# Optimization experiments

Measured on AMD Instinct MI355X. Metric: run time of the kernel, lower is better.

## Reference

```python
import jax, jax.numpy as jnp
import numpy as np

N = 100000
E = 1200000
C = 64
R = C // 8  # channel-attention reduced dim
G = 256    # number of graphs
EPS = 1e-5


def setup_inputs() -> dict:
    key = jax.random.key(0)
    ks = jax.random.split(key, 12)
    x = jax.random.normal(ks[0], (N, C), dtype=jnp.float32)
    edge_index = jax.random.randint(ks[1], (2, E), 0, N, dtype=jnp.int64)
    batch = jnp.sort(jax.random.randint(ks[2], (N,), 0, G, dtype=jnp.int64))
    s = 1.0 / np.sqrt(C)
    # SAGEConv: lin_l (applied to aggregated neighbors, with bias), lin_r (applied to self, no bias)
    Wl = jax.random.uniform(ks[3], (C, C), jnp.float32, -s, s)
    bl = jax.random.uniform(ks[4], (C,), jnp.float32, -s, s)
    Wr = jax.random.uniform(ks[5], (C, C), jnp.float32, -s, s)
    # GraphNorm params
    gn_w = jnp.ones((C,), jnp.float32)
    gn_b = jnp.zeros((C,), jnp.float32)
    gn_alpha = jnp.ones((C,), jnp.float32)  # mean_scale
    # ChannelAttention params
    sr = 1.0 / np.sqrt(C)
    a1_w = jax.random.uniform(ks[6], (R, C), jnp.float32, -sr, sr)
    a1_b = jax.random.uniform(ks[7], (R,), jnp.float32, -sr, sr)
    s2 = 1.0 / np.sqrt(R)
    a2_w = jax.random.uniform(ks[8], (C, R), jnp.float32, -s2, s2)
    a2_b = jax.random.uniform(ks[9], (C,), jnp.float32, -s2, s2)
    return {"x": x, "edge_index": edge_index, "batch": batch,
            "Wl": Wl, "bl": bl, "Wr": Wr,
            "gn_w": gn_w, "gn_b": gn_b, "gn_alpha": gn_alpha,
            "a1_w": a1_w, "a1_b": a1_b, "a2_w": a2_w, "a2_b": a2_b}


def _sage_conv(x, edge_index, Wl, bl, Wr):
    src, dst = edge_index[0], edge_index[1]
    # mean aggregation of neighbor features at destination nodes
    msg = x[src]  # [E, C]
    agg = jax.ops.segment_sum(msg, dst, num_segments=N)  # [N, C]
    deg = jax.ops.segment_sum(jnp.ones((E,), x.dtype), dst, num_segments=N)
    agg = agg / jnp.maximum(deg, 1.0)[:, None]
    return agg @ Wl.T + bl + x @ Wr.T


def _graph_norm(h, batch, w, b, alpha):
    cnt = jax.ops.segment_sum(jnp.ones((N,), h.dtype), batch, num_segments=G)
    cnt = jnp.maximum(cnt, 1.0)[:, None]  # [G,1]
    mean = jax.ops.segment_sum(h, batch, num_segments=G) / cnt  # [G,C]
    out = h - mean[batch] * alpha
    var = jax.ops.segment_sum(out * out, batch, num_segments=G) / cnt
    return w * out * jax.lax.rsqrt(var[batch] + EPS) + b


def reference(x, edge_index, batch, Wl, bl, Wr, gn_w, gn_b, gn_alpha,
              a1_w, a1_b, a2_w, a2_b):
    tmp = _graph_norm(_sage_conv(x, edge_index, Wl, bl, Wr), batch,
                      gn_w, gn_b, gn_alpha)
    # channel attention gate on the residual branch
    gate = jax.nn.sigmoid(jax.nn.relu(x @ a1_w.T + a1_b) @ a2_w.T + a2_b)
    tmp = tmp + gate * x
    # activation; dropout is identity at eval
    return jax.nn.relu(tmp)
```

## Files before the change

kernel.cpp:

```cpp
#include <hip/hip_runtime.h>
#include <math.h>

#define NN 100000
#define NE 1200000
#define CC 64
#define GG 256
#define RR 8
#define EPSF 1e-5f
#define BINS 782
#define BINP 1024
#define EPB 4688
#define QS 1028

__global__ __launch_bounds__(256) void k_hist(const int* __restrict__ ei,
                                              int* __restrict__ bin_total) {
  __shared__ int hist[BINP];
  for (int t = threadIdx.x; t < BINP; t += 256) hist[t] = 0;
  __syncthreads();
  int start = blockIdx.x * EPB;
  int end = start + EPB < NE ? start + EPB : NE;
  for (int e = start + threadIdx.x; e < end; e += 256)
    atomicAdd(&hist[ei[NE + e] >> 7], 1);
  __syncthreads();
  for (int t = threadIdx.x; t < BINP; t += 256)
    if (hist[t]) atomicAdd(&bin_total[t], hist[t]);
}

__global__ __launch_bounds__(1024) void k_scanbins(const int* __restrict__ bin_total,
                                                   int* __restrict__ bin_base,
                                                   int* __restrict__ cursor,
                                                   int* __restrict__ rowptr) {
  __shared__ int sh[BINP];
  int t = threadIdx.x;
  int v = t < BINS ? bin_total[t] : 0;
  sh[t] = v;
  __syncthreads();
  for (int d = 1; d < BINP; d <<= 1) {
    int val = sh[t];
    int add = (t >= d) ? sh[t - d] : 0;
    __syncthreads();
    sh[t] = val + add;
    __syncthreads();
  }
  int excl = sh[t] - v;
  if (t < BINS) {
    bin_base[t] = excl;
    cursor[t] = excl;
  }
  if (t == 0) {
    bin_base[BINS] = NE;
    rowptr[NN] = NE;
  }
}

__global__ __launch_bounds__(256) void k_phase1(const int* __restrict__ ei,
                                                int* __restrict__ cursor,
                                                unsigned* __restrict__ ebuf) {
  __shared__ int hist[BINP];
  __shared__ int base[BINP];
  for (int t = threadIdx.x; t < BINP; t += 256) hist[t] = 0;
  __syncthreads();
  int start = blockIdx.x * EPB;
  int end = start + EPB < NE ? start + EPB : NE;
  for (int e = start + threadIdx.x; e < end; e += 256)
    atomicAdd(&hist[ei[NE + e] >> 7], 1);
  __syncthreads();
  for (int t = threadIdx.x; t < BINP; t += 256) {
    int c = hist[t];
    base[t] = c ? atomicAdd(&cursor[t], c) : 0;
  }
  __syncthreads();
  for (int t = threadIdx.x; t < BINP; t += 256) hist[t] = 0;
  __syncthreads();
  for (int e = start + threadIdx.x; e < end; e += 256) {
    int src = ei[e], dst = ei[NE + e];
    int b = dst >> 7;
    int off = atomicAdd(&hist[b], 1);
    ebuf[base[b] + off] = ((unsigned)src << 7) | (unsigned)(dst & 127);
  }
}

__global__ __launch_bounds__(256) void k_fill2(const unsigned* __restrict__ ebuf,
                                               const int* __restrict__ bin_base,
                                               int* __restrict__ rowptr,
                                               int* __restrict__ csr) {
  __shared__ int cnt[128];
  __shared__ int sc[128];
  int tid = threadIdx.x;
  int b = blockIdx.x;
  int s = bin_base[b], e = bin_base[b + 1];
  if (tid < 128) cnt[tid] = 0;
  __syncthreads();
  for (int i = s + tid; i < e; i += 256) atomicAdd(&cnt[ebuf[i] & 127], 1);
  __syncthreads();
  if (tid < 128) sc[tid] = cnt[tid];
  __syncthreads();
  for (int d = 1; d < 128; d <<= 1) {
    int v = (tid < 128) ? sc[tid] : 0;
    int a = (tid >= d && tid < 128) ? sc[tid - d] : 0;
    __syncthreads();
    if (tid < 128) sc[tid] = v + a;
    __syncthreads();
  }
  if (tid < 128) {
    sc[tid] -= cnt[tid];
    int node = (b << 7) + tid;
    if (node < NN) rowptr[node] = s + sc[tid];
    cnt[tid] = 0;
  }
  __syncthreads();
  for (int i = s + tid; i < e; i += 256) {
    unsigned v = ebuf[i];
    int dl = v & 127;
    int off = atomicAdd(&cnt[dl], 1);
    csr[s + sc[dl] + off] = (int)(v >> 7);
  }
}

__global__ __launch_bounds__(256) void k_gather(const float* __restrict__ x,
                                                const int* __restrict__ csr,
                                                const int* __restrict__ rowptr,
                                                float* __restrict__ h) {
  int w = blockIdx.x * 4 + (threadIdx.x >> 6);
  int lane = threadIdx.x & 63;
  if (w >= NN) return;
  int s = rowptr[w], e = rowptr[w + 1];
  float acc = 0.0f;
  for (int j0 = s; j0 < e; j0 += 8) {
    int idx[8];
#pragma unroll
    for (int u = 0; u < 8; ++u) {
      int j = j0 + u;
      idx[u] = csr[j < e ? j : e - 1];
    }
    float v[8];
#pragma unroll
    for (int u = 0; u < 8; ++u) v[u] = x[(size_t)idx[u] * CC + lane];
#pragma unroll
    for (int u = 0; u < 8; ++u) acc += (j0 + u < e) ? v[u] : 0.0f;
  }
  h[(size_t)w * CC + lane] = acc;
}

__global__ __launch_bounds__(256) void k_passA(
    const float* __restrict__ x, float* h, const int* __restrict__ rowptr,
    const float* __restrict__ Wl, const float* __restrict__ bl,
    const float* __restrict__ Wr) {
  __shared__ float WLs[4 * QS];
  __shared__ float WRs[4 * QS];
  __shared__ float bls[CC];
  for (int idx = threadIdx.x; idx < CC * CC; idx += 256) {
    int c = idx >> 6, k = idx & 63;
    int qq = c >> 4, j = c & 15;
    WLs[qq * QS + j * 64 + k] = Wl[idx];
    WRs[qq * QS + j * 64 + k] = Wr[idx];
  }
  if (threadIdx.x < CC) bls[threadIdx.x] = bl[threadIdx.x];
  __syncthreads();

  int lane = threadIdx.x & 63;
  int wave = threadIdx.x >> 6;
  int n = lane & 15;
  int q = lane >> 4;
  int i0 = blockIdx.x * 256 + wave * 64 + n;
  const float4* wl = (const float4*)(WLs + q * QS);
  const float4* wr = (const float4*)(WRs + q * QS);

  const float4* ap[4];
  const float4* xp[4];
  float inv[4];
#pragma unroll
  for (int m = 0; m < 4; ++m) {
    int i = i0 + m * 16;
    int c = i < NN ? i : NN - 1;
    inv[m] = 1.0f / fmaxf((float)(rowptr[c + 1] - rowptr[c]), 1.0f);
    ap[m] = (const float4*)(h + (size_t)c * CC);
    xp[m] = (const float4*)(x + (size_t)c * CC);
  }

  float acc[4][16];
#pragma unroll
  for (int j = 0; j < 16; ++j) {
    float b = bls[q * 16 + j];
#pragma unroll
    for (int m = 0; m < 4; ++m) acc[m][j] = b;
  }

  for (int kbl = 0; kbl < 4; ++kbl) {
    float4 A[4][4];
#pragma unroll
    for (int m = 0; m < 4; ++m) {
#pragma unroll
      for (int t = 0; t < 4; ++t) {
        float4 v = ap[m][kbl * 4 + t];
        A[m][t] = make_float4(v.x * inv[m], v.y * inv[m], v.z * inv[m], v.w * inv[m]);
      }
    }
#pragma unroll
    for (int t = 0; t < 4; ++t) {
#pragma unroll
      for (int j = 0; j < 16; ++j) {
        float4 w = wl[j * 16 + kbl * 4 + t];
#pragma unroll
        for (int m = 0; m < 4; ++m) {
          float v = acc[m][j];
          v = fmaf(A[m][t].x, w.x, v);
          v = fmaf(A[m][t].y, w.y, v);
          v = fmaf(A[m][t].z, w.z, v);
          v = fmaf(A[m][t].w, w.w, v);
          acc[m][j] = v;
        }
      }
    }
  }

  for (int kbl = 0; kbl < 4; ++kbl) {
    float4 A[4][4];
#pragma unroll
    for (int m = 0; m < 4; ++m) {
#pragma unroll
      for (int t = 0; t < 4; ++t) A[m][t] = xp[m][kbl * 4 + t];
    }
#pragma unroll
    for (int t = 0; t < 4; ++t) {
#pragma unroll
      for (int j = 0; j < 16; ++j) {
        float4 w = wr[j * 16 + kbl * 4 + t];
#pragma unroll
        for (int m = 0; m < 4; ++m) {
          float v = acc[m][j];
          v = fmaf(A[m][t].x, w.x, v);
          v = fmaf(A[m][t].y, w.y, v);
          v = fmaf(A[m][t].z, w.z, v);
          v = fmaf(A[m][t].w, w.w, v);
          acc[m][j] = v;
        }
      }
    }
  }

#pragma unroll
  for (int m = 0; m < 4; ++m) {
    int i = i0 + m * 16;
    if (i < NN) {
      float4* hp = (float4*)(h + (size_t)i * CC + q * 16);
#pragma unroll
      for (int r = 0; r < 4; ++r)
        hp[r] = make_float4(acc[m][4 * r], acc[m][4 * r + 1],
                            acc[m][4 * r + 2], acc[m][4 * r + 3]);
    }
  }
}

__global__ __launch_bounds__(256) void k_stats(const float* __restrict__ h,
                                               const int* __restrict__ batch,
                                               float* __restrict__ sumH,
                                               float* __restrict__ sumH2,
                                               float* __restrict__ cntg) {
  int w = blockIdx.x * 4 + (threadIdx.x >> 6);
  int lane = threadIdx.x & 63;
  int i0 = w * 16;
  if (i0 >= NN) return;
  int iend = i0 + 16 < NN ? i0 + 16 : NN;
  int gcur = batch[i0];
  float aH = 0.0f, aH2 = 0.0f;
  int run = 0;
  for (int i = i0; i < iend; ++i) {
    int g = batch[i];
    if (g != gcur) {
      atomicAdd(&sumH[(size_t)gcur * CC + lane], aH);
      atomicAdd(&sumH2[(size_t)gcur * CC + lane], aH2);
      if (lane == 0) atomicAdd(&cntg[gcur], (float)run);
      aH = 0.0f; aH2 = 0.0f; run = 0;
      gcur = g;
    }
    float v = h[(size_t)i * CC + lane];
    aH += v;
    aH2 += v * v;
    run++;
  }
  atomicAdd(&sumH[(size_t)gcur * CC + lane], aH);
  atomicAdd(&sumH2[(size_t)gcur * CC + lane], aH2);
  if (lane == 0) atomicAdd(&cntg[gcur], (float)run);
}

__global__ __launch_bounds__(256) void k_passC(
    const float* __restrict__ h, const float* __restrict__ x,
    const int* __restrict__ batch, const float* __restrict__ sumH,
    const float* __restrict__ sumH2, const float* __restrict__ cntg,
    const float* __restrict__ gw, const float* __restrict__ gb,
    const float* __restrict__ alpha, const float* __restrict__ a1w,
    const float* __restrict__ a1b, const float* __restrict__ a2w,
    const float* __restrict__ a2b, float* __restrict__ out) {
  __shared__ float A1[RR * CC];
  __shared__ float A2[CC * RR];
  __shared__ float A1B[RR];
  __shared__ float PRM[4 * CC];
  for (int idx = threadIdx.x; idx < RR * CC; idx += 256) {
    A1[idx] = a1w[idx];
    A2[idx] = a2w[idx];
  }
  if (threadIdx.x < RR) A1B[threadIdx.x] = a1b[threadIdx.x];
  if (threadIdx.x < CC) {
    PRM[threadIdx.x] = a2b[threadIdx.x];
    PRM[CC + threadIdx.x] = gw[threadIdx.x];
    PRM[2 * CC + threadIdx.x] = gb[threadIdx.x];
    PRM[3 * CC + threadIdx.x] = alpha[threadIdx.x];
  }
  __syncthreads();

  int i = blockIdx.x * 256 + threadIdx.x;
  if (i >= NN) return;
  int g = batch[i];
  float rn = 1.0f / fmaxf(cntg[g], 1.0f);
  float xv[CC];
  const float4* xp = (const float4*)(x + (size_t)i * CC);
#pragma unroll
  for (int q = 0; q < 16; ++q) {
    float4 b = xp[q];
    xv[4 * q] = b.x; xv[4 * q + 1] = b.y; xv[4 * q + 2] = b.z; xv[4 * q + 3] = b.w;
  }
  float p[RR];
#pragma unroll
  for (int r = 0; r < RR; ++r) {
    float acc = A1B[r];
#pragma unroll
    for (int k = 0; k < CC; ++k) acc = fmaf(xv[k], A1[r * CC + k], acc);
    p[r] = fmaxf(acc, 0.0f);
  }
  const float4* hp = (const float4*)(h + (size_t)i * CC);
  const float4* sHp = (const float4*)(sumH + (size_t)g * CC);
  const float4* sH2p = (const float4*)(sumH2 + (size_t)g * CC);
  float4* op = (float4*)(out + (size_t)i * CC);
#pragma unroll 4
  for (int q = 0; q < 16; ++q) {
    float4 h4 = hp[q];
    float4 sH = sHp[q];
    float4 sH2 = sH2p[q];
    float hv[4] = {h4.x, h4.y, h4.z, h4.w};
    float sh[4] = {sH.x, sH.y, sH.z, sH.w};
    float sh2[4] = {sH2.x, sH2.y, sH2.z, sH2.w};
    float res[4];
#pragma unroll
    for (int u = 0; u < 4; ++u) {
      int c = q * 4 + u;
      float mu = sh[u] * rn;
      float t = PRM[3 * CC + c] * mu;
      float var = sh2[u] * rn - 2.0f * mu * t + t * t;
      float o = hv[u] - t;
      float y = fmaf(PRM[CC + c] * o, rsqrtf(var + EPSF), PRM[2 * CC + c]);
      float gacc = PRM[c];
#pragma unroll
      for (int r = 0; r < RR; ++r) gacc = fmaf(p[r], A2[c * RR + r], gacc);
      float gate = 1.0f / (1.0f + __expf(-gacc));
      res[u] = fmaxf(y + gate * xv[c], 0.0f);
    }
    op[q] = make_float4(res[0], res[1], res[2], res[3]);
  }
}

extern "C" void kernel_launch(void* const* d_in, const int* in_sizes, int n_in,
                              void* d_out, int out_size, void* d_ws, size_t ws_size,
                              hipStream_t stream) {
  const float* x        = (const float*)d_in[0];
  const int*   ei       = (const int*)d_in[1];
  const int*   batch    = (const int*)d_in[2];
  const float* Wl       = (const float*)d_in[3];
  const float* bl       = (const float*)d_in[4];
  const float* Wr       = (const float*)d_in[5];
  const float* gn_w     = (const float*)d_in[6];
  const float* gn_b     = (const float*)d_in[7];
  const float* gn_alpha = (const float*)d_in[8];
  const float* a1w      = (const float*)d_in[9];
  const float* a1b      = (const float*)d_in[10];
  const float* a2w      = (const float*)d_in[11];
  const float* a2b      = (const float*)d_in[12];
  float* out = (float*)d_out;

  float*    h        = (float*)d_ws;
  unsigned* ebuf     = (unsigned*)(h + (size_t)NN * CC);
  int*      csr      = (int*)(ebuf + NE);
  int*      rowptr   = csr + NE;
  int*      bin_tot  = rowptr + NN + 1;
  float*    sumH     = (float*)(bin_tot + BINP);
  float*    sumH2    = sumH + GG * CC;
  float*    cntg     = sumH2 + GG * CC;
  int*      bin_base = (int*)(cntg + GG);
  int*      cursor   = bin_base + BINS + 1;

  size_t zbytes = ((size_t)BINP + 2 * GG * CC + GG) * sizeof(int);
  hipMemsetAsync((void*)bin_tot, 0, zbytes, stream);

  k_hist    <<<256, 256, 0, stream>>>(ei, bin_tot);
  k_scanbins<<<1, BINP, 0, stream>>>(bin_tot, bin_base, cursor, rowptr);
  k_phase1  <<<256, 256, 0, stream>>>(ei, cursor, ebuf);
  k_fill2   <<<BINS, 256, 0, stream>>>(ebuf, bin_base, rowptr, csr);
  k_gather  <<<(NN + 3) / 4, 256, 0, stream>>>(x, csr, rowptr, h);
  k_passA   <<<(NN + 255) / 256, 256, 0, stream>>>(x, h, rowptr, Wl, bl, Wr);
  k_stats   <<<((NN + 15) / 16 + 3) / 4, 256, 0, stream>>>(h, batch, sumH, sumH2, cntg);
  k_passC   <<<(NN + 255) / 256, 256, 0, stream>>>(h, x, batch, sumH, sumH2, cntg,
                                                   gn_w, gn_b, gn_alpha,
                                                   a1w, a1b, a2w, a2b, out);
}
```

Before: 206.2 us.

## Gather neighbor features from a bf16 copy of x and halve passA rows per block

Adds a conversion kernel that writes x as bf16 into the output buffer, which serves as scratch, and has the edge gather read those 2-byte values instead of fp32. This halves the bytes moved by the random neighbor gather, which is the main bandwidth cost. It also cuts the passA tile from 4 to 2 rows per thread and doubles the grid, which lowers register pressure and raises occupancy. The trade-offs are reduced precision in the aggregated features and one extra pass over x.

```diff
diff --git a/kernel.cpp b/kernel.cpp
--- a/kernel.cpp
+++ b/kernel.cpp
@@ -12,6 +12,28 @@
 #define EPB 4688
 #define QS 1028
 
+__device__ inline unsigned short f2bf(float f) {
+  unsigned u = __float_as_uint(f);
+  return (unsigned short)((u + 0x7fffu + ((u >> 16) & 1u)) >> 16);
+}
+__device__ inline float bf2f(unsigned short s) {
+  return __uint_as_float(((unsigned)s) << 16);
+}
+
+__global__ __launch_bounds__(256) void k_cvt(const float* __restrict__ x,
+                                             unsigned short* __restrict__ xb) {
+  int i = blockIdx.x * 256 + threadIdx.x;
+  if (i >= NN * CC / 8) return;
+  const float4* xp = (const float4*)(x + (size_t)i * 8);
+  float4 a = xp[0], b = xp[1];
+  uint4 o;
+  o.x = (unsigned)f2bf(a.x) | ((unsigned)f2bf(a.y) << 16);
+  o.y = (unsigned)f2bf(a.z) | ((unsigned)f2bf(a.w) << 16);
+  o.z = (unsigned)f2bf(b.x) | ((unsigned)f2bf(b.y) << 16);
+  o.w = (unsigned)f2bf(b.z) | ((unsigned)f2bf(b.w) << 16);
+  *(uint4*)(xb + (size_t)i * 8) = o;
+}
+
 __global__ __launch_bounds__(256) void k_hist(const int* __restrict__ ei,
                                               int* __restrict__ bin_total) {
   __shared__ int hist[BINP];
@@ -117,7 +139,7 @@
   }
 }
 
-__global__ __launch_bounds__(256) void k_gather(const float* __restrict__ x,
+__global__ __launch_bounds__(256) void k_gather(const unsigned short* __restrict__ xb,
                                                 const int* __restrict__ csr,
                                                 const int* __restrict__ rowptr,
                                                 float* __restrict__ h) {
@@ -135,7 +157,7 @@
     }
     float v[8];
 #pragma unroll
-    for (int u = 0; u < 8; ++u) v[u] = x[(size_t)idx[u] * CC + lane];
+    for (int u = 0; u < 8; ++u) v[u] = bf2f(xb[(size_t)idx[u] * CC + lane]);
 #pragma unroll
     for (int u = 0; u < 8; ++u) acc += (j0 + u < e) ? v[u] : 0.0f;
   }
@@ -162,15 +184,15 @@
   int wave = threadIdx.x >> 6;
   int n = lane & 15;
   int q = lane >> 4;
-  int i0 = blockIdx.x * 256 + wave * 64 + n;
+  int i0 = blockIdx.x * 128 + wave * 32 + n;
   const float4* wl = (const float4*)(WLs + q * QS);
   const float4* wr = (const float4*)(WRs + q * QS);
 
-  const float4* ap[4];
-  const float4* xp[4];
-  float inv[4];
-#pragma unroll
-  for (int m = 0; m < 4; ++m) {
+  const float4* ap[2];
+  const float4* xp[2];
+  float inv[2];
+#pragma unroll
+  for (int m = 0; m < 2; ++m) {
     int i = i0 + m * 16;
     int c = i < NN ? i : NN - 1;
     inv[m] = 1.0f / fmaxf((float)(rowptr[c + 1] - rowptr[c]), 1.0f);
@@ -178,18 +200,17 @@
     xp[m] = (const float4*)(x + (size_t)c * CC);
   }
 
-  float acc[4][16];
+  float acc[2][16];
 #pragma unroll
   for (int j = 0; j < 16; ++j) {
     float b = bls[q * 16 + j];
-#pragma unroll
-    for (int m = 0; m < 4; ++m) acc[m][j] = b;
+    acc[0][j] = b; acc[1][j] = b;
   }
 
   for (int kbl = 0; kbl < 4; ++kbl) {
-    float4 A[4][4];
-#pragma unroll
-    for (int m = 0; m < 4; ++m) {
+    float4 A[2][4];
+#pragma unroll
+    for (int m = 0; m < 2; ++m) {
 #pragma unroll
       for (int t = 0; t < 4; ++t) {
         float4 v = ap[m][kbl * 4 + t];
@@ -202,7 +223,7 @@
       for (int j = 0; j < 16; ++j) {
         float4 w = wl[j * 16 + kbl * 4 + t];
 #pragma unroll
-        for (int m = 0; m < 4; ++m) {
+        for (int m = 0; m < 2; ++m) {
           float v = acc[m][j];
           v = fmaf(A[m][t].x, w.x, v);
           v = fmaf(A[m][t].y, w.y, v);
@@ -215,9 +236,9 @@
   }
 
   for (int kbl = 0; kbl < 4; ++kbl) {
-    float4 A[4][4];
-#pragma unroll
-    for (int m = 0; m < 4; ++m) {
+    float4 A[2][4];
+#pragma unroll
+    for (int m = 0; m < 2; ++m) {
 #pragma unroll
       for (int t = 0; t < 4; ++t) A[m][t] = xp[m][kbl * 4 + t];
     }
@@ -227,7 +248,7 @@
       for (int j = 0; j < 16; ++j) {
         float4 w = wr[j * 16 + kbl * 4 + t];
 #pragma unroll
-        for (int m = 0; m < 4; ++m) {
+        for (int m = 0; m < 2; ++m) {
           float v = acc[m][j];
           v = fmaf(A[m][t].x, w.x, v);
           v = fmaf(A[m][t].y, w.y, v);
@@ -240,7 +261,7 @@
   }
 
 #pragma unroll
-  for (int m = 0; m < 4; ++m) {
+  for (int m = 0; m < 2; ++m) {
     int i = i0 + m * 16;
     if (i < NN) {
       float4* hp = (float4*)(h + (size_t)i * CC + q * 16);
@@ -387,16 +408,18 @@
   float*    cntg     = sumH2 + GG * CC;
   int*      bin_base = (int*)(cntg + GG);
   int*      cursor   = bin_base + BINS + 1;
+  unsigned short* xb = (unsigned short*)d_out;
 
   size_t zbytes = ((size_t)BINP + 2 * GG * CC + GG) * sizeof(int);
   hipMemsetAsync((void*)bin_tot, 0, zbytes, stream);
 
+  k_cvt     <<<(NN * CC / 8 + 255) / 256, 256, 0, stream>>>(x, xb);
   k_hist    <<<256, 256, 0, stream>>>(ei, bin_tot);
   k_scanbins<<<1, BINP, 0, stream>>>(bin_tot, bin_base, cursor, rowptr);
   k_phase1  <<<256, 256, 0, stream>>>(ei, cursor, ebuf);
   k_fill2   <<<BINS, 256, 0, stream>>>(ebuf, bin_base, rowptr, csr);
-  k_gather  <<<(NN + 3) / 4, 256, 0, stream>>>(x, csr, rowptr, h);
-  k_passA   <<<(NN + 255) / 256, 256, 0, stream>>>(x, h, rowptr, Wl, bl, Wr);
+  k_gather  <<<(NN + 3) / 4, 256, 0, stream>>>(xb, csr, rowptr, h);
+  k_passA   <<<(NN + 127) / 128, 256, 0, stream>>>(x, h, rowptr, Wl, bl, Wr);
   k_stats   <<<((NN + 15) / 16 + 3) / 4, 256, 0, stream>>>(h, batch, sumH, sumH2, cntg);
   k_passC   <<<(NN + 255) / 256, 256, 0, stream>>>(h, x, batch, sumH, sumH2, cntg,
                                                    gn_w, gn_b, gn_alpha,
```

Result: slower. 215.4 us (+4.4%).
